# Optimization experiments

Measured on AMD Instinct MI355X. Metric: run time of the kernel, lower is better.

## Reference

```python
import jax, jax.numpy as jnp
import numpy as np

EMBEDDING_DIM = 1024


def setup_inputs() -> dict:
    key = jax.random.key(0)
    x = jax.random.normal(key, (8, 4096, EMBEDDING_DIM), dtype=jnp.float32)
    return {"x": x}


def reference(x):
    # x: [B, S, D]. pe[pos, i] = sin(pos / 10000**((i//2)/S)) if i even else cos(...)
    # NOTE: faithful to source: exponent denominator is len_sequence S, not D.
    S = x.shape[1]
    D = x.shape[2]
    pos = jnp.arange(S, dtype=jnp.float32)[:, None]            # [S, 1]
    i = jnp.arange(D)                                          # [D]
    k = (i // 2).astype(jnp.float32)[None, :]                  # [1, D]
    angle = pos / jnp.power(jnp.float32(10000.0), k / jnp.float32(S))  # [S, D]
    pe = jnp.where((i % 2 == 0)[None, :], jnp.sin(angle), jnp.cos(angle))
    return x + pe[None, :, :].astype(x.dtype)
```

## Files before the change

kernel.cpp:

```cpp
#include <hip/hip_runtime.h>


#define PE_S 4096
#define PE_D 1024
#define N4   (8 * PE_S * PE_D / 4)

typedef float f32x4 __attribute__((ext_vector_type(4)));

__global__ __launch_bounds__(256) void PositionalEncoding_84095459656362_kernel(
    const float* __restrict__ x, float* __restrict__ out) {
    const int i  = blockIdx.x * blockDim.x + threadIdx.x;
    const int d4 = (i & (PE_D / 4 - 1)) << 2;
    const int s  = (i >> 8) & (PE_S - 1);

    const float c   = -0.0032440703857f;
    const float r1  = 0.99775390625f;
    const float e0  = __builtin_exp2f((float)(d4 >> 1) * c);
    const float a0  = (float)s * e0;
    const float a1  = a0 * r1;

    float s0, c0, s1, c1;
    __sincosf(a0, &s0, &c0);
    __sincosf(a1, &s1, &c1);

    const f32x4 v = ((const f32x4*)x)[i];
    f32x4 r;
    r.x = v.x + s0;
    r.y = v.y + c0;
    r.z = v.z + s1;
    r.w = v.w + c1;
    ((f32x4*)out)[i] = r;
}

extern "C" void kernel_launch(void* const* d_in, const int* in_sizes, int n_in,
                              void* d_out, int out_size, void* d_ws, size_t ws_size,
                              hipStream_t stream) {
    const float* x = (const float*)d_in[0];
    float* out = (float*)d_out;
    PositionalEncoding_84095459656362_kernel<<<N4 / 256, 256, 0, stream>>>(x, out);
}
```

Baseline: 220.1 us.

## Use persistent grid-stride loop reusing positional encodings across batches

Launches a fixed grid of 2048 blocks, each covering two sequence positions (s and s+2048), so the positional encoding values are computed once per thread and reused across all 8 batches. Each thread then loops over the batch with software-pipelined loads (prefetching the next pair before storing the current). This removes redundant transcendental work and reduces block launch count, at the cost of fewer, longer-lived threads, which may lower memory-level parallelism on a purely bandwidth-bound kernel.

```diff
diff --git a/kernel.cpp b/kernel.cpp
--- a/kernel.cpp
+++ b/kernel.cpp
@@ -1,35 +1,56 @@
 #include <hip/hip_runtime.h>
 
 
-#define PE_S 4096
-#define PE_D 1024
-#define N4   (8 * PE_S * PE_D / 4)
+#define PE_S    4096
+#define PE_D    1024
+#define N4      (8 * PE_S * PE_D / 4)
+#define BLOCKS  2048
+#define THREADS 256
+#define STRIDE  (BLOCKS * THREADS)
+#define ITERS   (N4 / STRIDE)
 
 typedef float f32x4 __attribute__((ext_vector_type(4)));
 
-__global__ __launch_bounds__(256) void PositionalEncoding_84095459656362_kernel(
+__global__ __launch_bounds__(THREADS, 8) void PositionalEncoding_84095459656362_kernel(
     const float* __restrict__ x, float* __restrict__ out) {
-    const int i  = blockIdx.x * blockDim.x + threadIdx.x;
-    const int d4 = (i & (PE_D / 4 - 1)) << 2;
-    const int s  = (i >> 8) & (PE_S - 1);
+    const int i0 = blockIdx.x * THREADS + threadIdx.x;
+    const int d4 = (i0 & (PE_D / 4 - 1)) << 2;
+    const int s0 = i0 >> 8;
 
-    const float c   = -0.0032440703857f;
-    const float r1  = 0.99775390625f;
-    const float e0  = __builtin_exp2f((float)(d4 >> 1) * c);
-    const float a0  = (float)s * e0;
-    const float a1  = a0 * r1;
+    const float c  = -0.0032440703857f;
+    const float r1 = 0.99775390625f;
+    const float e0 = __builtin_exp2f((float)(d4 >> 1) * c);
 
-    float s0, c0, s1, c1;
-    __sincosf(a0, &s0, &c0);
-    __sincosf(a1, &s1, &c1);
+    const float ae0 = (float)s0 * e0;
+    const float ae1 = ae0 * r1;
+    const float ao0 = (float)(s0 + 2048) * e0;
+    const float ao1 = ao0 * r1;
 
-    const f32x4 v = ((const f32x4*)x)[i];
-    f32x4 r;
-    r.x = v.x + s0;
-    r.y = v.y + c0;
-    r.z = v.z + s1;
-    r.w = v.w + c1;
-    ((f32x4*)out)[i] = r;
+    float sa, ca, sb, cb;
+    f32x4 pe0, pe1;
+    __sincosf(ae0, &sa, &ca);
+    __sincosf(ae1, &sb, &cb);
+    pe0.x = sa; pe0.y = ca; pe0.z = sb; pe0.w = cb;
+    __sincosf(ao0, &sa, &ca);
+    __sincosf(ao1, &sb, &cb);
+    pe1.x = sa; pe1.y = ca; pe1.z = sb; pe1.w = cb;
+
+    const f32x4* xin = (const f32x4*)x + i0;
+    f32x4*       o   = (f32x4*)out     + i0;
+
+    f32x4 v0 = xin[0];
+    f32x4 v1 = xin[STRIDE];
+#pragma unroll
+    for (int k = 0; k < ITERS - 2; k += 2) {
+        const f32x4 n0 = xin[(k + 2) * STRIDE];
+        const f32x4 n1 = xin[(k + 3) * STRIDE];
+        o[k * STRIDE]       = v0 + pe0;
+        o[(k + 1) * STRIDE] = v1 + pe1;
+        v0 = n0;
+        v1 = n1;
+    }
+    o[(ITERS - 2) * STRIDE] = v0 + pe0;
+    o[(ITERS - 1) * STRIDE] = v1 + pe1;
 }
 
 extern "C" void kernel_launch(void* const* d_in, const int* in_sizes, int n_in,
@@ -37,5 +58,5 @@
                               hipStream_t stream) {
     const float* x = (const float*)d_in[0];
     float* out = (float*)d_out;
-    PositionalEncoding_84095459656362_kernel<<<N4 / 256, 256, 0, stream>>>(x, out);
+    PositionalEncoding_84095459656362_kernel<<<BLOCKS, THREADS, 0, stream>>>(x, out);
 }
```

Result: slower. 244.1 us (+10.9%).
